# Kernel tuning notes

Hardware: AMD Instinct MI355X
Metric: run time of the kernel (lower is better)

## Reference

```python
import jax, jax.numpy as jnp
import numpy as np

B, S, E, H = 4, 2048, 1024, 16
D = E // H  # head dim = 64


def setup_inputs() -> dict:
    key = jax.random.key(0)
    ks = jax.random.split(key, 8)
    scale = 0.02
    return {
        "query": jax.random.normal(ks[0], (B, S, E), jnp.float32),
        "keys": jax.random.normal(ks[1], (B, S, E), jnp.float32),
        "values": jax.random.normal(ks[2], (B, S, E), jnp.float32),
        "mask": jnp.ones((B, 1, 1, S), jnp.int32),
        "Wq": jax.random.normal(ks[3], (D, D), jnp.float32) * scale,
        "Wk": jax.random.normal(ks[4], (D, D), jnp.float32) * scale,
        "Wv": jax.random.normal(ks[5], (D, D), jnp.float32) * scale,
        "Wf": jax.random.normal(ks[6], (E, E), jnp.float32) * scale,
        "bf": jax.random.normal(ks[7], (E,), jnp.float32) * scale,
    }


def reference(query, keys, values, mask, Wq, Wk, Wv, Wf, bf):
    b, sq, _ = query.shape
    sk = keys.shape[1]
    # reshape to heads: [b, s, H, D]
    q = query.reshape(b, sq, H, D)
    k = keys.reshape(b, sk, H, D)
    v = values.reshape(b, sk, H, D)
    # per-head linear projections (torch Linear: x @ W.T, no bias)
    q = jnp.einsum('bshd,ed->bshe', q, Wq)
    k = jnp.einsum('bshd,ed->bshe', k, Wk)
    v = jnp.einsum('bshd,ed->bshe', v, Wv)
    # scores [b, h, q, k]
    scores = jnp.einsum('bqhd,bkhd->bhqk', q, k)
    scores = jnp.where(mask == 0, -jnp.inf, scores)
    attn = jax.nn.softmax(scores / jnp.sqrt(jnp.float32(D)), axis=3)
    # context [b, q, h, d] -> [b, q, E]
    ctx = jnp.einsum('bhqk,bkhd->bqhd', attn, v).reshape(b, sq, E)
    return ctx @ Wf.T + bf
```

## Files before the change

kernel.cpp:

```cpp
#include <hip/hip_runtime.h>

#define B_ 4
#define S_ 2048
#define E_ 1024
#define H_ 16
#define D_ 64

typedef unsigned short u16;
typedef unsigned int u32;
typedef __bf16 bf16x8 __attribute__((ext_vector_type(8)));
typedef float f32x4 __attribute__((ext_vector_type(4)));
typedef u16 u16x8 __attribute__((ext_vector_type(8)));
typedef u16 u16x4 __attribute__((ext_vector_type(4)));

#if defined(__has_builtin)
#if __has_builtin(__builtin_amdgcn_exp2f)
#define EXP2F(x) __builtin_amdgcn_exp2f(x)
#else
#define EXP2F(x) exp2f(x)
#endif
#else
#define EXP2F(x) exp2f(x)
#endif

__device__ __forceinline__ u16 bfbits(float f) {
  __bf16 h = (__bf16)f;
  return __builtin_bit_cast(u16, h);
}
__device__ __forceinline__ f32x4 mfma16(bf16x8 a, bf16x8 b, f32x4 c) {
  return __builtin_amdgcn_mfma_f32_16x16x32_bf16(a, b, c, 0, 0, 0);
}
__device__ __forceinline__ bf16x8 lds_ld8(const u16* base, int off) {
  return *reinterpret_cast<const bf16x8*>(reinterpret_cast<const char*>(base) + off);
}
__device__ __forceinline__ void gload_lds16(const u16* g, u16* l) {
  __builtin_amdgcn_global_load_lds((const __attribute__((address_space(1))) void*)g,
                                   (__attribute__((address_space(3))) void*)l, 16, 0, 0);
}

__global__ __launch_bounds__(256) void proj_kernel(
    const float* __restrict__ qin, const float* __restrict__ kin, const float* __restrict__ vin,
    const float* __restrict__ Wq, const float* __restrict__ Wk, const float* __restrict__ Wv,
    const float* __restrict__ Wf,
    u16* __restrict__ qo, u16* __restrict__ ko, u16* __restrict__ vo, u16* __restrict__ wfo)
{
  const int t = threadIdx.x;
  const int tensor = blockIdx.z >> 2, b = blockIdx.z & 3;

  if (tensor == 3) {
    int chunk = ((blockIdx.z & 3) * 16 + blockIdx.y) * 16 + blockIdx.x;
    int i = chunk * 256 + t;
    float4 f = reinterpret_cast<const float4*>(Wf)[i];
    u16x4 h4;
    h4[0] = bfbits(f.x); h4[1] = bfbits(f.y); h4[2] = bfbits(f.z); h4[3] = bfbits(f.w);
    reinterpret_cast<u16x4*>(wfo)[i] = h4;
    return;
  }

  __shared__ __align__(16) u16 Al[128 * 64];
  __shared__ __align__(16) u16 Wl[64 * 64];
  const int w = t >> 6, l = t & 63, lg = l >> 4, ln = l & 15;
  const int h = blockIdx.y, s0 = blockIdx.x * 128;

  const float* x; const float* W; float scale;
  if (tensor == 0)      { x = qin; W = Wq; scale = 0.125f * 1.44269504f; }
  else if (tensor == 1) { x = kin; W = Wk; scale = 1.0f; }
  else                  { x = vin; W = Wv; scale = 1.0f; }

  {
    const int e = t >> 2, d0 = (t & 3) * 16;
    const float4* wr = reinterpret_cast<const float4*>(W + e * 64 + d0);
    float4 f0 = wr[0], f1 = wr[1], f2 = wr[2], f3 = wr[3];
    u16x8 p0, p1;
    p0[0]=bfbits(f0.x*scale); p0[1]=bfbits(f0.y*scale); p0[2]=bfbits(f0.z*scale); p0[3]=bfbits(f0.w*scale);
    p0[4]=bfbits(f1.x*scale); p0[5]=bfbits(f1.y*scale); p0[6]=bfbits(f1.z*scale); p0[7]=bfbits(f1.w*scale);
    p1[0]=bfbits(f2.x*scale); p1[1]=bfbits(f2.y*scale); p1[2]=bfbits(f2.z*scale); p1[3]=bfbits(f2.w*scale);
    p1[4]=bfbits(f3.x*scale); p1[5]=bfbits(f3.y*scale); p1[6]=bfbits(f3.z*scale); p1[7]=bfbits(f3.w*scale);
    *reinterpret_cast<u16x8*>(reinterpret_cast<char*>(Wl) + ((e*128 + d0*2     ) ^ ((e & 7) << 4))) = p0;
    *reinterpret_cast<u16x8*>(reinterpret_cast<char*>(Wl) + ((e*128 + d0*2 + 16) ^ ((e & 7) << 4))) = p1;
  }
  {
    const int row = t >> 1, d0 = (t & 1) * 32;
    const float4* xr = reinterpret_cast<const float4*>(x + ((size_t)(b * S_ + s0 + row)) * E_ + h * D_ + d0);
    #pragma unroll
    for (int c = 0; c < 4; ++c) {
      float4 f0 = xr[2 * c], f1 = xr[2 * c + 1];
      u16x8 pk;
      pk[0]=bfbits(f0.x); pk[1]=bfbits(f0.y); pk[2]=bfbits(f0.z); pk[3]=bfbits(f0.w);
      pk[4]=bfbits(f1.x); pk[5]=bfbits(f1.y); pk[6]=bfbits(f1.z); pk[7]=bfbits(f1.w);
      *reinterpret_cast<u16x8*>(reinterpret_cast<char*>(Al) +
          ((row * 128 + (d0 + 8 * c) * 2) ^ ((row & 7) << 4))) = pk;
    }
  }
  __syncthreads();

  bf16x8 wb[4][2];
  #pragma unroll
  for (int nn = 0; nn < 4; ++nn) {
    int brow = nn * 16 + ln;
    int bo = (brow * 128 + lg * 16) ^ ((ln & 7) << 4);
    wb[nn][0] = lds_ld8(Wl, bo);
    wb[nn][1] = lds_ld8(Wl, bo ^ 64);
  }
  f32x4 acc[2][4] = {};
  #pragma unroll
  for (int sub = 0; sub < 2; ++sub) {
    int arow = 32 * w + 16 * sub + ln;
    int ao = (arow * 128 + lg * 16) ^ ((ln & 7) << 4);
    bf16x8 a0 = lds_ld8(Al, ao), a1 = lds_ld8(Al, ao ^ 64);
    #pragma unroll
    for (int nn = 0; nn < 4; ++nn) {
      acc[sub][nn] = mfma16(a0, wb[nn][0], acc[sub][nn]);
      acc[sub][nn] = mfma16(a1, wb[nn][1], acc[sub][nn]);
    }
  }

  if (tensor < 2) {
    u16* o = (tensor == 0) ? qo : ko;
    const size_t hb = ((size_t)(b * H_ + h)) * (S_ * D_);
    #pragma unroll
    for (int sub = 0; sub < 2; ++sub)
      #pragma unroll
      for (int nn = 0; nn < 4; ++nn)
        #pragma unroll
        for (int r = 0; r < 4; ++r)
          o[hb + (size_t)(s0 + 32*w + 16*sub + 4*lg + r) * D_ + nn*16 + ln] = bfbits(acc[sub][nn][r]);
  } else {
    const size_t hb = ((size_t)(b * H_ + h)) * (D_ * S_);
    #pragma unroll
    for (int sub = 0; sub < 2; ++sub)
      #pragma unroll
      for (int nn = 0; nn < 4; ++nn)
        #pragma unroll
        for (int r = 0; r < 4; ++r) {
          int scol = s0 + 32*w + 16*sub + 4*lg + r;
          int sl = scol & 63;
          int c = (sl & 3) | (((sl >> 4) & 1) << 2) | (((sl >> 2) & 3) << 3) | ((sl >> 5) << 5);
          vo[hb + (size_t)(nn*16 + ln) * S_ + (scol & ~63) + c] = bfbits(acc[sub][nn][r]);
        }
  }
}

__global__ __launch_bounds__(512, 4) void attn_kernel(
    const u16* __restrict__ qw,
    const u16* __restrict__ kw,
    const u16* __restrict__ vtw,
    const int* __restrict__ mask,
    u16* __restrict__ ctx)
{
  __shared__ __align__(16) u16 Kl[2][64 * 64];
  __shared__ __align__(16) u16 Vl[2][64 * 64];
  __shared__ int s_allone;

  const int t = threadIdx.x, w = t >> 6, l = t & 63, lg = l >> 4, ln = l & 15;
  const int hb = blockIdx.x;
  const int b = hb >> 4;
  const int q0 = blockIdx.y * 256;
  const size_t koff = (size_t)hb * (S_ * D_);
  const size_t voff = (size_t)hb * (D_ * S_);

  if (t == 0) s_allone = 1;
  __syncthreads();

  const int srow = t >> 3, scol = (t & 7) ^ ((t >> 3) & 7);
  const u16* kg = kw + koff + srow * D_ + scol * 8;
  const u16* vg = vtw + voff + (size_t)srow * S_ + scol * 8;
  u16* kd = &Kl[0][0] + t * 8;
  u16* vd = &Vl[0][0] + t * 8;

  gload_lds16(kg, kd);
  gload_lds16(vg, vd);

  {
    const int4 m4 = *reinterpret_cast<const int4*>(mask + b * S_ + t * 4);
    if (!(m4.x && m4.y && m4.z && m4.w)) s_allone = 0;
  }

  bf16x8 qb[2][2];
  #pragma unroll
  for (int sub = 0; sub < 2; ++sub) {
    const u16* qp = qw + koff + (size_t)(q0 + 32*w + 16*sub + ln) * D_ + 8*lg;
    qb[sub][0] = *reinterpret_cast<const bf16x8*>(qp);
    qb[sub][1] = *reinterpret_cast<const bf16x8*>(qp + 32);
  }

  u16x8 ob;
  #pragma unroll
  for (int i = 0; i < 8; ++i) ob[i] = 0x3F80;
  const bf16x8 ones = __builtin_bit_cast(bf16x8, ob);

  f32x4 oacc[2][4] = {};
  f32x4 lacc[2] = {};

  asm volatile("s_waitcnt vmcnt(0)" ::: "memory");
  __syncthreads();
  const int allone = s_allone;

  int cur = 0;
  for (int kt = 0; kt < S_ / 64; ++kt) {
    if (kt + 1 < S_ / 64) {
      const int nk = (kt + 1) * 64;
      gload_lds16(kg + nk * D_, kd + (cur ^ 1) * 4096);
      gload_lds16(vg + nk,      vd + (cur ^ 1) * 4096);
    }
    const u16* Kc = &Kl[cur][0];
    const u16* Vc = &Vl[cur][0];

    f32x4 sc[2][4];
    __builtin_amdgcn_s_setprio(1);
    #pragma unroll
    for (int kn = 0; kn < 4; ++kn) {
      int o0 = ((ln * 128 + lg * 16) ^ ((ln & 7) << 4)) + kn * 2048;
      bf16x8 ka0 = lds_ld8(Kc, o0), ka1 = lds_ld8(Kc, o0 ^ 64);
      #pragma unroll
      for (int sub = 0; sub < 2; ++sub) {
        f32x4 z = {0.f, 0.f, 0.f, 0.f};
        z = mfma16(ka0, qb[sub][0], z);
        z = mfma16(ka1, qb[sub][1], z);
        sc[sub][kn] = z;
      }
    }
    __builtin_amdgcn_s_setprio(0);

    if (!allone) {
      const int kv0 = kt * 64;
      #pragma unroll
      for (int kn = 0; kn < 4; ++kn) {
        const int4 m4 = *reinterpret_cast<const int4*>(mask + b * S_ + kv0 + kn * 16 + lg * 4);
        const int* mp = reinterpret_cast<const int*>(&m4);
        #pragma unroll
        for (int r = 0; r < 4; ++r)
          if (mp[r] == 0) { sc[0][kn][r] = -1e30f; sc[1][kn][r] = -1e30f; }
      }
    }

    bf16x8 pa[2][2];
    #pragma unroll
    for (int sub = 0; sub < 2; ++sub)
      #pragma unroll
      for (int kn = 0; kn < 4; ++kn)
        #pragma unroll
        for (int r = 0; r < 4; ++r)
          pa[sub][kn >> 1][(kn & 1) * 4 + r] = (__bf16)EXP2F(sc[sub][kn][r]);

    __builtin_amdgcn_s_setprio(1);
    #pragma unroll
    for (int sub = 0; sub < 2; ++sub) {
      lacc[sub] = mfma16(pa[sub][0], ones, lacc[sub]);
      lacc[sub] = mfma16(pa[sub][1], ones, lacc[sub]);
    }
    #pragma unroll
    for (int kh = 0; kh < 2; ++kh)
      #pragma unroll
      for (int dn = 0; dn < 4; ++dn) {
        int vo0 = ((ln * 128 + 16 * lg + 64 * kh) ^ ((ln & 7) << 4)) + dn * 2048;
        bf16x8 vb = lds_ld8(Vc, vo0);
        #pragma unroll
        for (int sub = 0; sub < 2; ++sub)
          oacc[sub][dn] = mfma16(pa[sub][kh], vb, oacc[sub][dn]);
      }
    __builtin_amdgcn_s_setprio(0);

    if (kt + 1 < S_ / 64) {
      asm volatile("s_waitcnt vmcnt(0)" ::: "memory");
      __syncthreads();
      cur ^= 1;
    }
  }

  #pragma unroll
  for (int sub = 0; sub < 2; ++sub) {
    #pragma unroll
    for (int r = 0; r < 4; ++r) {
      float linv = 1.f / lacc[sub][r];
      int qrow = q0 + 32 * w + 16 * sub + 4 * lg + r;
      size_t base = ((size_t)b * S_ + qrow) * E_ + (hb & 15) * D_;
      #pragma unroll
      for (int dn = 0; dn < 4; ++dn)
        ctx[base + dn * 16 + ln] = bfbits(oacc[sub][dn][r] * linv);
    }
  }
}

__global__ __launch_bounds__(256, 2) void outproj_kernel(
    const u16* __restrict__ ctx, const u16* __restrict__ wf,
    const float* __restrict__ bias, float* __restrict__ out)
{
  __shared__ __align__(16) u16 Al[2][128 * 64];
  __shared__ __align__(16) u16 Bl[2][128 * 64];
  const int t = threadIdx.x, w = t >> 6, l = t & 63, lg = l >> 4, ln = l & 15;
  const int wm = w >> 1, wn = w & 1;
  const int m0 = blockIdx.x * 128, n0 = blockIdx.y * 128;
  f32x4 acc[4][4] = {};

  const u16* ag[4]; const u16* bg[4]; int ldo[4];
  #pragma unroll
  for (int it = 0; it < 4; ++it) {
    int j = it * 256 + t, row = j >> 3, c = (j & 7) ^ (row & 7);
    ag[it] = ctx + (size_t)(m0 + row) * E_ + c * 8;
    bg[it] = wf  + (size_t)(n0 + row) * E_ + c * 8;
    ldo[it] = j * 8;
  }
  #pragma unroll
  for (int it = 0; it < 4; ++it) {
    gload_lds16(ag[it], &Al[0][0] + ldo[it]);
    gload_lds16(bg[it], &Bl[0][0] + ldo[it]);
  }
  asm volatile("s_waitcnt vmcnt(0)" ::: "memory");
  __syncthreads();

  int cur = 0;
  for (int kt = 0; kt < E_ / 64; ++kt) {
    if (kt + 1 < E_ / 64) {
      const int k0 = (kt + 1) * 64;
      #pragma unroll
      for (int it = 0; it < 4; ++it) {
        gload_lds16(ag[it] + k0, &Al[cur ^ 1][0] + ldo[it]);
        gload_lds16(bg[it] + k0, &Bl[cur ^ 1][0] + ldo[it]);
      }
    }
    const u16* Ac = &Al[cur][0]; const u16* Bc = &Bl[cur][0];

    bf16x8 af[4][2], bff[4][2];
    #pragma unroll
    for (int ms = 0; ms < 4; ++ms) {
      int ar = 64 * wm + 16 * ms + ln;
      int ao = (ar * 128 + lg * 16) ^ ((ln & 7) << 4);
      af[ms][0] = lds_ld8(Ac, ao); af[ms][1] = lds_ld8(Ac, ao ^ 64);
    }
    #pragma unroll
    for (int ns = 0; ns < 4; ++ns) {
      int br = 64 * wn + 16 * ns + ln;
      int bo = (br * 128 + lg * 16) ^ ((ln & 7) << 4);
      bff[ns][0] = lds_ld8(Bc, bo); bff[ns][1] = lds_ld8(Bc, bo ^ 64);
    }
    __builtin_amdgcn_s_setprio(1);
    #pragma unroll
    for (int ms = 0; ms < 4; ++ms)
      #pragma unroll
      for (int ns = 0; ns < 4; ++ns) {
        acc[ms][ns] = mfma16(af[ms][0], bff[ns][0], acc[ms][ns]);
        acc[ms][ns] = mfma16(af[ms][1], bff[ns][1], acc[ms][ns]);
      }
    __builtin_amdgcn_s_setprio(0);

    if (kt + 1 < E_ / 64) {
      asm volatile("s_waitcnt vmcnt(0)" ::: "memory");
      __syncthreads();
      cur ^= 1;
    }
  }

  #pragma unroll
  for (int ns = 0; ns < 4; ++ns) {
    float bv = bias[n0 + 64 * wn + 16 * ns + ln];
    #pragma unroll
    for (int ms = 0; ms < 4; ++ms)
      #pragma unroll
      for (int r = 0; r < 4; ++r)
        out[(size_t)(m0 + 64*wm + 16*ms + 4*lg + r) * E_ + n0 + 64*wn + 16*ns + ln] =
            acc[ms][ns][r] + bv;
  }
}

extern "C" void kernel_launch(void* const* d_in, const int* in_sizes, int n_in,
                              void* d_out, int out_size, void* d_ws, size_t ws_size,
                              hipStream_t stream)
{
  const float* q   = (const float*)d_in[0];
  const float* k   = (const float*)d_in[1];
  const float* v   = (const float*)d_in[2];
  const int*  mask = (const int*) d_in[3];
  const float* Wq  = (const float*)d_in[4];
  const float* Wk  = (const float*)d_in[5];
  const float* Wv  = (const float*)d_in[6];
  const float* Wf  = (const float*)d_in[7];
  const float* bfv = (const float*)d_in[8];
  float* out = (float*)d_out;

  const size_t NQKV = (size_t)B_ * H_ * S_ * D_;
  const size_t NCTX = (size_t)B_ * S_ * E_;
  u16* q_ws   = (u16*)d_ws;
  u16* k_ws   = q_ws + NQKV;
  u16* v_ws   = k_ws + NQKV;
  u16* ctx_ws = v_ws + NQKV;
  u16* wf_ws  = ctx_ws + NCTX;

  proj_kernel<<<dim3(S_ / 128, H_, 16), dim3(256), 0, stream>>>(
      q, k, v, Wq, Wk, Wv, Wf, q_ws, k_ws, v_ws, wf_ws);
  attn_kernel<<<dim3(B_ * H_, S_ / 256), dim3(512), 0, stream>>>(
      q_ws, k_ws, v_ws, mask, ctx_ws);
  outproj_kernel<<<dim3((B_ * S_) / 128, E_ / 128), dim3(256), 0, stream>>>(
      ctx_ws, wf_ws, bfv, out);
}
```

Before: 120.5 us.

## Software-pipeline attention loop: overlap QK of next tile with exp/PV of previous

Restructures the attention main loop into a two-stage software pipeline. Each iteration computes QK scores for the current KV tile while doing the mask, exp and PV accumulation for the previous tile, using ping-pong score registers and V fragments preloaded into registers before the barrier. The loop is manually unrolled by two so buffer indices are compile-time constants. Occupancy hint drops from 4 to 2 blocks per CU to allow the extra registers, which risks less latency hiding across waves.

```diff
diff --git a/kernel.cpp b/kernel.cpp
--- a/kernel.cpp
+++ b/kernel.cpp
@@ -141,7 +141,90 @@
   }
 }
 
-__global__ __launch_bounds__(512, 4) void attn_kernel(
+#define QK_PHASE(SCW)                                                          \
+  {                                                                            \
+    __builtin_amdgcn_s_setprio(1);                                             \
+    _Pragma("unroll")                                                          \
+    for (int kn = 0; kn < 4; ++kn) {                                           \
+      int o0 = ((ln * 128 + lg * 16) ^ ((ln & 7) << 4)) + kn * 2048;           \
+      bf16x8 ka0 = lds_ld8(Kc, o0), ka1 = lds_ld8(Kc, o0 ^ 64);                \
+      _Pragma("unroll")                                                        \
+      for (int sub = 0; sub < 2; ++sub) {                                      \
+        f32x4 z = {0.f, 0.f, 0.f, 0.f};                                        \
+        z = mfma16(ka0, qb[sub][0], z);                                        \
+        z = mfma16(ka1, qb[sub][1], z);                                        \
+        SCW[sub][kn] = z;                                                      \
+      }                                                                        \
+    }                                                                          \
+    __builtin_amdgcn_s_setprio(0);                                             \
+  }
+
+#define EXPPV_PHASE(SCR, KV0PREV)                                              \
+  {                                                                            \
+    if (!allone) {                                                             \
+      const int kv0p = (KV0PREV);                                              \
+      _Pragma("unroll")                                                        \
+      for (int kn = 0; kn < 4; ++kn) {                                         \
+        const int4 m4 = *reinterpret_cast<const int4*>(                        \
+            mask + b * S_ + kv0p + kn * 16 + lg * 4);                          \
+        const int* mp = reinterpret_cast<const int*>(&m4);                     \
+        _Pragma("unroll")                                                      \
+        for (int r = 0; r < 4; ++r)                                            \
+          if (mp[r] == 0) { SCR[0][kn][r] = -1e30f; SCR[1][kn][r] = -1e30f; }  \
+      }                                                                        \
+    }                                                                          \
+    bf16x8 pa[2][2];                                                           \
+    _Pragma("unroll")                                                          \
+    for (int sub = 0; sub < 2; ++sub)                                          \
+      _Pragma("unroll")                                                        \
+      for (int kn = 0; kn < 4; ++kn)                                           \
+        _Pragma("unroll")                                                      \
+        for (int r = 0; r < 4; ++r)                                            \
+          pa[sub][kn >> 1][(kn & 1) * 4 + r] = (__bf16)EXP2F(SCR[sub][kn][r]); \
+    __builtin_amdgcn_s_setprio(1);                                             \
+    _Pragma("unroll")                                                          \
+    for (int sub = 0; sub < 2; ++sub) {                                        \
+      lacc[sub] = mfma16(pa[sub][0], ones, lacc[sub]);                         \
+      lacc[sub] = mfma16(pa[sub][1], ones, lacc[sub]);                         \
+    }                                                                          \
+    _Pragma("unroll")                                                          \
+    for (int kh = 0; kh < 2; ++kh)                                             \
+      _Pragma("unroll")                                                        \
+      for (int dn = 0; dn < 4; ++dn)                                           \
+        _Pragma("unroll")                                                      \
+        for (int sub = 0; sub < 2; ++sub)                                      \
+          oacc[sub][dn] = mfma16(pa[sub][kh], vf[kh][dn], oacc[sub][dn]);      \
+    __builtin_amdgcn_s_setprio(0);                                             \
+  }
+
+#define VREAD_PHASE                                                            \
+  _Pragma("unroll")                                                            \
+  for (int kh = 0; kh < 2; ++kh)                                               \
+    _Pragma("unroll")                                                          \
+    for (int dn = 0; dn < 4; ++dn) {                                           \
+      int vo0 = ((ln * 128 + 16 * lg + 64 * kh) ^ ((ln & 7) << 4)) + dn * 2048;\
+      vf[kh][dn] = lds_ld8(Vc, vo0);                                           \
+    }
+
+#define ATTN_ITER(KT, SCW, SCR, CUR, LAST)                                     \
+  {                                                                            \
+    const u16* Kc = &Kl[CUR][0];                                               \
+    const u16* Vc = &Vl[CUR][0];                                               \
+    if (!(LAST)) {                                                             \
+      const int nk = ((KT) + 1) * 64;                                          \
+      gload_lds16(kg + nk * D_, kd + ((CUR) ^ 1) * 4096);                      \
+      gload_lds16(vg + nk,      vd + ((CUR) ^ 1) * 4096);                      \
+    }                                                                          \
+    QK_PHASE(SCW)                                                              \
+    EXPPV_PHASE(SCR, ((KT) - 1) * 64)                                          \
+    VREAD_PHASE                                                                \
+    if (!(LAST)) {                                                             \
+      asm volatile("s_waitcnt vmcnt(0)" ::: "memory");                         \
+      __syncthreads();                                                         \
+    }                                                                          \
+  }
+
+__global__ __launch_bounds__(512, 2) void attn_kernel(
     const u16* __restrict__ qw,
     const u16* __restrict__ kw,
     const u16* __restrict__ vtw,
@@ -191,82 +274,30 @@
 
   f32x4 oacc[2][4] = {};
   f32x4 lacc[2] = {};
+  f32x4 scA[2][4], scB[2][4];
+  bf16x8 vf[2][4];
 
   asm volatile("s_waitcnt vmcnt(0)" ::: "memory");
   __syncthreads();
   const int allone = s_allone;
 
-  int cur = 0;
-  for (int kt = 0; kt < S_ / 64; ++kt) {
-    if (kt + 1 < S_ / 64) {
-      const int nk = (kt + 1) * 64;
-      gload_lds16(kg + nk * D_, kd + (cur ^ 1) * 4096);
-      gload_lds16(vg + nk,      vd + (cur ^ 1) * 4096);
-    }
-    const u16* Kc = &Kl[cur][0];
-    const u16* Vc = &Vl[cur][0];
-
-    f32x4 sc[2][4];
-    __builtin_amdgcn_s_setprio(1);
-    #pragma unroll
-    for (int kn = 0; kn < 4; ++kn) {
-      int o0 = ((ln * 128 + lg * 16) ^ ((ln & 7) << 4)) + kn * 2048;
-      bf16x8 ka0 = lds_ld8(Kc, o0), ka1 = lds_ld8(Kc, o0 ^ 64);
-      #pragma unroll
-      for (int sub = 0; sub < 2; ++sub) {
-        f32x4 z = {0.f, 0.f, 0.f, 0.f};
-        z = mfma16(ka0, qb[sub][0], z);
-        z = mfma16(ka1, qb[sub][1], z);
-        sc[sub][kn] = z;
-      }
-    }
-    __builtin_amdgcn_s_setprio(0);
-
-    if (!allone) {
-      const int kv0 = kt * 64;
-      #pragma unroll
-      for (int kn = 0; kn < 4; ++kn) {
-        const int4 m4 = *reinterpret_cast<const int4*>(mask + b * S_ + kv0 + kn * 16 + lg * 4);
-        const int* mp = reinterpret_cast<const int*>(&m4);
-        #pragma unroll
-        for (int r = 0; r < 4; ++r)
-          if (mp[r] == 0) { sc[0][kn][r] = -1e30f; sc[1][kn][r] = -1e30f; }
-      }
-    }
-
-    bf16x8 pa[2][2];
-    #pragma unroll
-    for (int sub = 0; sub < 2; ++sub)
-      #pragma unroll
-      for (int kn = 0; kn < 4; ++kn)
-        #pragma unroll
-        for (int r = 0; r < 4; ++r)
-          pa[sub][kn >> 1][(kn & 1) * 4 + r] = (__bf16)EXP2F(sc[sub][kn][r]);
-
-    __builtin_amdgcn_s_setprio(1);
-    #pragma unroll
-    for (int sub = 0; sub < 2; ++sub) {
-      lacc[sub] = mfma16(pa[sub][0], ones, lacc[sub]);
-      lacc[sub] = mfma16(pa[sub][1], ones, lacc[sub]);
-    }
-    #pragma unroll
-    for (int kh = 0; kh < 2; ++kh)
-      #pragma unroll
-      for (int dn = 0; dn < 4; ++dn) {
-        int vo0 = ((ln * 128 + 16 * lg + 64 * kh) ^ ((ln & 7) << 4)) + dn * 2048;
-        bf16x8 vb = lds_ld8(Vc, vo0);
-        #pragma unroll
-        for (int sub = 0; sub < 2; ++sub)
-          oacc[sub][dn] = mfma16(pa[sub][kh], vb, oacc[sub][dn]);
-      }
-    __builtin_amdgcn_s_setprio(0);
-
-    if (kt + 1 < S_ / 64) {
-      asm volatile("s_waitcnt vmcnt(0)" ::: "memory");
-      __syncthreads();
-      cur ^= 1;
-    }
-  }
+  {
+    const u16* Kc = &Kl[0][0];
+    const u16* Vc = &Vl[0][0];
+    gload_lds16(kg + 64 * D_, kd + 4096);
+    gload_lds16(vg + 64,      vd + 4096);
+    QK_PHASE(scA)
+    VREAD_PHASE
+    asm volatile("s_waitcnt vmcnt(0)" ::: "memory");
+    __syncthreads();
+  }
+
+  for (int kt = 1; kt < 31; kt += 2) {
+    ATTN_ITER(kt,     scB, scA, 1, false)
+    ATTN_ITER(kt + 1, scA, scB, 0, false)
+  }
+  ATTN_ITER(31, scB, scA, 1, true)
+  EXPPV_PHASE(scB, 31 * 64)
 
   #pragma unroll
   for (int sub = 0; sub < 2; ++sub) {
```

Result: slower. 127.9 us (+6.1%).
